# Kernel optimization log

Hardware: AMD Instinct MI355X
Metric: run time of the kernel (lower is better)

## Reference

```python
import jax, jax.numpy as jnp
import numpy as np

S = 4096          # number of samples
N_NODES = 2048    # sum nodes in this layer
N_CHILD = 4096    # nodes per child layer
NNZ = 32768       # nonzeros per sparse log-weight matrix


def setup_inputs() -> dict:
    key = jax.random.key(0)
    ks = jax.random.split(key, 8)
    ll0 = jax.random.normal(ks[0], (S, N_CHILD), dtype=jnp.float32)
    ll1 = jax.random.normal(ks[1], (S, N_CHILD), dtype=jnp.float32)
    w0_data = jax.random.normal(ks[2], (NNZ,), dtype=jnp.float32)
    w1_data = jax.random.normal(ks[3], (NNZ,), dtype=jnp.float32)
    w0_rows = jax.random.randint(ks[4], (NNZ,), 0, N_NODES, dtype=jnp.int32)
    w0_cols = jax.random.randint(ks[5], (NNZ,), 0, N_CHILD, dtype=jnp.int32)
    w1_rows = jax.random.randint(ks[6], (NNZ,), 0, N_NODES, dtype=jnp.int32)
    w1_cols = jax.random.randint(ks[7], (NNZ,), 0, N_CHILD, dtype=jnp.int32)
    return {"ll0": ll0, "ll1": ll1,
            "w0_data": w0_data, "w1_data": w1_data,
            "w0_rows": w0_rows, "w0_cols": w0_cols,
            "w1_rows": w1_rows, "w1_cols": w1_cols,
            "n_nodes": N_NODES}


def _sparse_weighted_sum(ll, data, rows, cols, n_nodes):
    # exp(ll) @ exp(W).T for BCOO W with shape (n_nodes, n_child)
    # contrib[s, k] = exp(ll[s, cols[k]]) * exp(data[k]); scatter-add over rows.
    contrib = jnp.exp(ll[:, cols] + data[None, :])  # (S, NNZ)
    return jnp.zeros((ll.shape[0], n_nodes), dtype=ll.dtype).at[:, rows].add(contrib)


def reference(ll0, ll1, w0_data, w1_data, w0_rows, w0_cols, w1_rows, w1_cols, n_nodes):
    # accumulate exp(ll_i) @ exp(W_i).T over child layers
    result = _sparse_weighted_sum(ll0, w0_data, w0_rows, w0_cols, n_nodes)
    result = result + _sparse_weighted_sum(ll1, w1_data, w1_rows, w1_cols, n_nodes)
    # log normalization constants: log(sum_j exp(concatenated log_weights)[i, j])
    z = jnp.zeros((n_nodes,), dtype=result.dtype)
    z = z.at[w0_rows].add(jnp.exp(w0_data))
    z = z.at[w1_rows].add(jnp.exp(w1_data))
    return jnp.log(result) - jnp.log(z)[None, :]
```

## Files before the change

kernel.cpp:

```cpp
#include <hip/hip_runtime.h>
#include <math.h>

#define S 4096
#define N_NODES 2048
#define N_CHILD 4096
#define NNZ 32768
#define NNZ_TOTAL (2 * NNZ)
#define TSM 512
#define TN 8
#define CAP 96
#define LP 516

typedef float f32x2 __attribute__((ext_vector_type(2)));


__global__ __launch_bounds__(1024, 8) void prep_kernel(
        const float* __restrict__ ll0, const float* __restrict__ ll1,
        const float* __restrict__ w0d, const float* __restrict__ w1d,
        const int* __restrict__ w0r, const int* __restrict__ w0c,
        const int* __restrict__ w1r, const int* __restrict__ w1c,
        unsigned char* __restrict__ ET, int2* __restrict__ ent,
        int* __restrict__ counts) {
    __shared__ unsigned short tile[64 * 130];
    int t = threadIdx.x;
    int b = blockIdx.x;
    if (b < 64) {
        int k = b * 1024 + t;
        int row, col; float w;
        if (k < NNZ) { row = w0r[k]; col = w0c[k]; w = w0d[k]; }
        else { int kk = k - NNZ; row = w1r[kk]; col = w1c[kk] + N_CHILD; w = w1d[kk]; }
        int pos = atomicAdd(&counts[row], 1);
        if (pos < CAP)
            ent[row * CAP + pos] = make_int2(col, __float_as_int(__expf(w)));
        return;
    }
    int bt = b - 64;
    int slice = bt & 7;
    int sthalf = (bt >> 3) & 1;
    int ct = (bt >> 4) & 63;
    int z = (bt >> 10) & 1;
    int c0 = ct * 64;
    int s0 = slice * 512 + sthalf * 256;
    const float* ll = z ? ll1 : ll0;
    int wave = t >> 6, lane = t & 63;
    float v0[8], v1[8];
    const float* p = ll + (size_t)(s0 + wave * 2) * N_CHILD + c0 + lane;
#pragma unroll
    for (int it = 0; it < 8; ++it) {
        v0[it] = p[0];
        v1[it] = p[N_CHILD];
        p += 32 * (size_t)N_CHILD;
    }
#pragma unroll
    for (int it = 0; it < 8; ++it) {
        int sh = it * 16 + wave;
        unsigned int packed = (unsigned int)__builtin_amdgcn_cvt_pk_fp8_f32(
            __expf(v0[it]), __expf(v1[it]), 0, false);
        tile[lane * 130 + sh] = (unsigned short)packed;
    }
    __syncthreads();
    unsigned char* dst = ET + (size_t)(z * N_CHILD + c0) * S + s0;
#pragma unroll
    for (int it = 0; it < 4; ++it) {
        int c = it * 16 + wave;
        unsigned int v = *(const unsigned int*)&tile[c * 130 + lane * 2];
        *(unsigned int*)(dst + (size_t)c * S + lane * 4) = v;
    }
}


static __device__ inline void fma16(uint4 x, float w, float* a) {
#pragma unroll
    for (int q = 0; q < 4; ++q) {
        unsigned int word = (q == 0) ? x.x : (q == 1) ? x.y : (q == 2) ? x.z : x.w;
        f32x2 lo = __builtin_amdgcn_cvt_pk_f32_fp8(word, false);
        f32x2 hi = __builtin_amdgcn_cvt_pk_f32_fp8(word, true);
        a[q * 4 + 0] = fmaf(lo.x, w, a[q * 4 + 0]);
        a[q * 4 + 1] = fmaf(lo.y, w, a[q * 4 + 1]);
        a[q * 4 + 2] = fmaf(hi.x, w, a[q * 4 + 2]);
        a[q * 4 + 3] = fmaf(hi.y, w, a[q * 4 + 3]);
    }
}

__global__ __launch_bounds__(256, 8) void main_kernel(
        const unsigned char* __restrict__ ET, const int2* __restrict__ ent,
        const int* __restrict__ counts, float* __restrict__ out) {
    __shared__ float lds[TN * LP];
    int t = threadIdx.x, wave = t >> 6, lane = t & 63;
    int hs = lane >> 5, sl = lane & 31;
    int slice = blockIdx.x & 7;
    int nb = blockIdx.x >> 3;
    int i0 = nb * TN;
    const unsigned char* ETs = ET + slice * TSM + sl * 16;
    for (int jj = 0; jj < 2; ++jj) {
        int j = wave * 2 + jj;
        int i = i0 + j;
        int cnt = __builtin_amdgcn_readfirstlane(counts[i]);
        if (cnt > CAP) cnt = CAP;
        const int2* eb = ent + i * CAP;
        float a[16];
#pragma unroll
        for (int u = 0; u < 16; ++u) a[u] = 0.f;
        float z = 0.f;
        int n = (cnt + 1 - hs) >> 1;
        int t2 = 0;
        for (; t2 + 1 < n; t2 += 2) {
            int2 e0 = eb[hs + 2 * t2];
            int2 e1 = eb[hs + 2 * t2 + 2];
            uint4 x0 = *(const uint4*)(ETs + (size_t)e0.x * S);
            uint4 x1 = *(const uint4*)(ETs + (size_t)e1.x * S);
            float w0 = __uint_as_float(e0.y);
            float w1 = __uint_as_float(e1.y);
            fma16(x0, w0, a);
            fma16(x1, w1, a);
            z += w0 + w1;
        }
        if (t2 < n) {
            int2 e0 = eb[hs + 2 * t2];
            uint4 x0 = *(const uint4*)(ETs + (size_t)e0.x * S);
            float w0 = __uint_as_float(e0.y);
            fma16(x0, w0, a);
            z += w0;
        }
#pragma unroll
        for (int u = 0; u < 16; ++u) a[u] += __shfl_xor(a[u], 32);
        z += __shfl_xor(z, 32);
        float lz = __logf(z);
        float r[8];
#pragma unroll
        for (int u = 0; u < 8; ++u) r[u] = __logf(a[hs * 8 + u]) - lz;
        float* dstl = &lds[j * LP + sl * 16 + hs * 8];
        *(float4*)(dstl)     = make_float4(r[0], r[1], r[2], r[3]);
        *(float4*)(dstl + 4) = make_float4(r[4], r[5], r[6], r[7]);
    }
    __syncthreads();
    float* obase = out + (size_t)slice * TSM * N_NODES + i0;
#pragma unroll
    for (int q = 0; q < 8; ++q) {
        int elem = (t + 256 * q) * 2;
        int s_l = elem >> 3;
        int i_l = elem & 7;
        float2 v;
        v.x = lds[i_l * LP + s_l];
        v.y = lds[(i_l + 1) * LP + s_l];
        *(float2*)&obase[(size_t)s_l * N_NODES + i_l] = v;
    }
}


extern "C" void kernel_launch(void* const* d_in, const int* in_sizes, int n_in,
                              void* d_out, int out_size, void* d_ws, size_t ws_size,
                              hipStream_t stream) {
    const float* ll0 = (const float*)d_in[0];
    const float* ll1 = (const float*)d_in[1];
    const float* w0d = (const float*)d_in[2];
    const float* w1d = (const float*)d_in[3];
    const int*   w0r = (const int*)d_in[4];
    const int*   w0c = (const int*)d_in[5];
    const int*   w1r = (const int*)d_in[6];
    const int*   w1c = (const int*)d_in[7];
    float* out = (float*)d_out;

    unsigned char* ET = (unsigned char*)d_ws;
    int2* ent   = (int2*)(ET + (size_t)2 * N_CHILD * S);
    int*  counts = (int*)(ent + (size_t)N_NODES * CAP);

    hipMemsetAsync(counts, 0, sizeof(int) * N_NODES, stream);
    prep_kernel<<<2112, 1024, 0, stream>>>(ll0, ll1, w0d, w1d, w0r, w0c, w1r, w1c,
                                           ET, ent, counts);
    main_kernel<<<(N_NODES / TN) * (S / TSM), 256, 0, stream>>>(ET, ent, counts, out);
}
```

Before: 222.0 us.

## Preload sparse entries into registers and broadcast via shuffles, unroll gather by four

Each wave now loads a row's sparse entry list once into registers (two int2 per lane) and pulls each entry out with lane shuffles. Previously every iteration issued a dependent global load for the entry before the gather. The main loop is unrolled to four gathers in flight. Out-of-range entries are masked to a zero weight with a clamped column, and the launch-bounds occupancy hint is lowered from 8 to 4 to leave room for more registers. It also adds a sched_barrier in the prep kernel and nontemporal output stores; the trade-off is extra shuffle instructions and lower occupancy.

New measurement: 229.4 us. 3.3% more time.

```diff
diff --git a/kernel.cpp b/kernel.cpp
--- a/kernel.cpp
+++ b/kernel.cpp
@@ -51,6 +51,7 @@
         v1[it] = p[N_CHILD];
         p += 32 * (size_t)N_CHILD;
     }
+    __builtin_amdgcn_sched_barrier(0);
 #pragma unroll
     for (int it = 0; it < 8; ++it) {
         int sh = it * 16 + wave;
@@ -82,7 +83,17 @@
     }
 }
 
-__global__ __launch_bounds__(256, 8) void main_kernel(
+static __device__ inline void entry_get(int t2, int hs, int cnt, int2 eA, int2 eB,
+                                        int& col, float& w) {
+    int k = hs + 2 * t2;
+    int c, wi;
+    if (t2 < 32) { c = __shfl(eA.x, k); wi = __shfl(eA.y, k); }
+    else         { c = __shfl(eB.x, k - 64); wi = __shfl(eB.y, k - 64); }
+    col = c & (2 * N_CHILD - 1);
+    w = (k < cnt) ? __uint_as_float(wi) : 0.f;
+}
+
+__global__ __launch_bounds__(256, 4) void main_kernel(
         const unsigned char* __restrict__ ET, const int2* __restrict__ ent,
         const int* __restrict__ counts, float* __restrict__ out) {
     __shared__ float lds[TN * LP];
@@ -98,27 +109,32 @@
         int cnt = __builtin_amdgcn_readfirstlane(counts[i]);
         if (cnt > CAP) cnt = CAP;
         const int2* eb = ent + i * CAP;
+        int2 eA = eb[lane];
+        int2 eB = eb[64 + (lane & 31)];
         float a[16];
 #pragma unroll
         for (int u = 0; u < 16; ++u) a[u] = 0.f;
         float z = 0.f;
-        int n = (cnt + 1 - hs) >> 1;
+        int nmax = (cnt + 1) >> 1;
         int t2 = 0;
-        for (; t2 + 1 < n; t2 += 2) {
-            int2 e0 = eb[hs + 2 * t2];
-            int2 e1 = eb[hs + 2 * t2 + 2];
-            uint4 x0 = *(const uint4*)(ETs + (size_t)e0.x * S);
-            uint4 x1 = *(const uint4*)(ETs + (size_t)e1.x * S);
-            float w0 = __uint_as_float(e0.y);
-            float w1 = __uint_as_float(e1.y);
-            fma16(x0, w0, a);
-            fma16(x1, w1, a);
-            z += w0 + w1;
+        for (; t2 + 3 < nmax; t2 += 4) {
+            int c0i, c1i, c2i, c3i; float w0, w1, w2, w3;
+            entry_get(t2 + 0, hs, cnt, eA, eB, c0i, w0);
+            entry_get(t2 + 1, hs, cnt, eA, eB, c1i, w1);
+            entry_get(t2 + 2, hs, cnt, eA, eB, c2i, w2);
+            entry_get(t2 + 3, hs, cnt, eA, eB, c3i, w3);
+            uint4 x0 = *(const uint4*)(ETs + (size_t)c0i * S);
+            uint4 x1 = *(const uint4*)(ETs + (size_t)c1i * S);
+            uint4 x2 = *(const uint4*)(ETs + (size_t)c2i * S);
+            uint4 x3 = *(const uint4*)(ETs + (size_t)c3i * S);
+            fma16(x0, w0, a); fma16(x1, w1, a);
+            fma16(x2, w2, a); fma16(x3, w3, a);
+            z += w0 + w1 + w2 + w3;
         }
-        if (t2 < n) {
-            int2 e0 = eb[hs + 2 * t2];
-            uint4 x0 = *(const uint4*)(ETs + (size_t)e0.x * S);
-            float w0 = __uint_as_float(e0.y);
+        for (; t2 < nmax; ++t2) {
+            int c0i; float w0;
+            entry_get(t2, hs, cnt, eA, eB, c0i, w0);
+            uint4 x0 = *(const uint4*)(ETs + (size_t)c0i * S);
             fma16(x0, w0, a);
             z += w0;
         }
@@ -140,10 +156,10 @@
         int elem = (t + 256 * q) * 2;
         int s_l = elem >> 3;
         int i_l = elem & 7;
-        float2 v;
+        f32x2 v;
         v.x = lds[i_l * LP + s_l];
         v.y = lds[(i_l + 1) * LP + s_l];
-        *(float2*)&obase[(size_t)s_l * N_NODES + i_l] = v;
+        __builtin_nontemporal_store(v, (f32x2*)&obase[(size_t)s_l * N_NODES + i_l]);
     }
 }
 
```
